# Performance work log

Measured on AMD Instinct MI355X. Metric: run time of the kernel, lower is better.

Reference implementation:

```python
import jax, jax.numpy as jnp
import numpy as np

B = 16
PATCH_NUM = 32      # L of inter branch
PATCH_SIZE = 128    # L of intra branch
WIN_SIZE = PATCH_NUM * PATCH_SIZE  # 4096
H = 8
E = 64


def setup_inputs() -> dict:
    key = jax.random.key(0)
    ks = jax.random.split(key, 6)
    return {
        "q_inter": jax.random.normal(ks[0], (B, PATCH_NUM, H, E), jnp.float32),
        "k_inter": jax.random.normal(ks[1], (B, PATCH_NUM, H, E), jnp.float32),
        "v_inter": jax.random.normal(ks[2], (B, PATCH_NUM, H, E), jnp.float32),
        "q_intra": jax.random.normal(ks[3], (B, PATCH_SIZE, H, E), jnp.float32),
        "k_intra": jax.random.normal(ks[4], (B, PATCH_SIZE, H, E), jnp.float32),
        "v_intra": jax.random.normal(ks[5], (B, PATCH_SIZE, H, E), jnp.float32),
    }


def _full_attention(q, k, v):
    # q,k,v: [B, L, H, E]; full softmax attention, scale = 1/sqrt(E)
    scale = 1.0 / jnp.sqrt(jnp.asarray(q.shape[-1], q.dtype))
    score = jnp.einsum('blhe,bshe->bhls', q, k) * scale
    att = jax.nn.softmax(score, axis=-1)  # dropout is identity in eval mode
    return jnp.einsum('bhls,bshd->blhd', att, v)


def reference(q_inter, k_inter, v_inter, q_intra, k_intra, v_intra):
    V_inter = _full_attention(q_inter, k_inter, v_inter)  # [B, patch_num, H, E]
    V_intra = _full_attention(q_intra, k_intra, v_intra)  # [B, patch_size, H, E]
    # einops repeat 'b pn h d -> b (pn ps) h d': each patch repeated ps times
    V_inter_up = jnp.repeat(V_inter, PATCH_SIZE, axis=1)  # [B, win_size, H, E]
    # einops repeat 'b ps h d -> b (ps pn) h d': each position repeated pn times
    V_intra_up = jnp.repeat(V_intra, PATCH_NUM, axis=1)   # [B, win_size, H, E]
    return V_inter_up + V_intra_up
```

## Files before the change

### kernel.cpp

```cpp
#include <hip/hip_runtime.h>


#define NH 8
#define NE 64
#define ROWSTRIDE (NH * NE)

__device__ __forceinline__ float dot4(const float4 a, const float4 b) {
    return a.x * b.x + a.y * b.y + a.z * b.z + a.w * b.w;
}

template <int L>
__global__ __launch_bounds__(256) void attn_kernel(
    const float* __restrict__ qg_, const float* __restrict__ kg_,
    const float* __restrict__ vg_, float* __restrict__ dst)
{
    constexpr int TILES = L / 32;
    constexpr int CPT   = L / 32;
    constexpr int SST   = L + 1;
    constexpr int KST   = 68;

    __shared__ __align__(16) float Ks[L * KST];
    __shared__ __align__(16) float Vs[L * KST];
    __shared__ __align__(16) float Qs[32 * KST];
    __shared__ float S[32 * SST];

    const int tid  = threadIdx.x;
    const int bid  = blockIdx.x;
    const int tile = bid % TILES;
    const int h    = (bid / TILES) % NH;
    const int b    = bid / (TILES * NH);
    const int r0   = tile * 32;

    const float* kg = kg_ + ((size_t)b * L * NH + h) * NE;
    const float* vg = vg_ + ((size_t)b * L * NH + h) * NE;
    const float* qg = qg_ + ((size_t)(b * L + r0) * NH + h) * NE;

    for (int idx = tid; idx < L * 16; idx += 256) {
        const int row = idx >> 4;
        const int f   = (idx & 15) * 4;
        *(float4*)&Ks[row * KST + f] = *(const float4*)(kg + (size_t)row * ROWSTRIDE + f);
        *(float4*)&Vs[row * KST + f] = *(const float4*)(vg + (size_t)row * ROWSTRIDE + f);
    }
    for (int idx = tid; idx < 32 * 16; idx += 256) {
        const int row = idx >> 4;
        const int f   = (idx & 15) * 4;
        *(float4*)&Qs[row * KST + f] = *(const float4*)(qg + (size_t)row * ROWSTRIDE + f);
    }
    __syncthreads();

    {
        const int rg = tid >> 5;
        const int cg = tid & 31;
        const int rr = rg * 4;
        const int c0 = cg * CPT;
        float acc[4][CPT];
        #pragma unroll
        for (int i = 0; i < 4; i++)
            #pragma unroll
            for (int j = 0; j < CPT; j++) acc[i][j] = 0.f;

        #pragma unroll
        for (int e = 0; e < NE; e += 4) {
            float4 qv[4], kv[CPT];
            #pragma unroll
            for (int i = 0; i < 4; i++) qv[i] = *(const float4*)&Qs[(rr + i) * KST + e];
            #pragma unroll
            for (int j = 0; j < CPT; j++) kv[j] = *(const float4*)&Ks[(c0 + j) * KST + e];
            #pragma unroll
            for (int i = 0; i < 4; i++)
                #pragma unroll
                for (int j = 0; j < CPT; j++)
                    acc[i][j] += dot4(qv[i], kv[j]);
        }
        #pragma unroll
        for (int i = 0; i < 4; i++)
            #pragma unroll
            for (int j = 0; j < CPT; j++)
                S[(rr + i) * SST + c0 + j] = acc[i][j] * 0.125f;
    }
    __syncthreads();

    const int r   = tid >> 3;
    const int sub = tid & 7;
    float m = -1e30f;
    for (int c = 0; c < L; c++) m = fmaxf(m, S[r * SST + c]);
    float sum = 0.f;
    for (int c = 0; c < L; c++) sum += __expf(S[r * SST + c] - m);
    const float inv = 1.f / sum;
    __syncthreads();
    for (int c = sub; c < L; c += 8)
        S[r * SST + c] = __expf(S[r * SST + c] - m);
    __syncthreads();

    const int e0 = sub * 8;
    float a0=0,a1=0,a2=0,a3=0,a4=0,a5=0,a6=0,a7=0;
    for (int c = 0; c < L; c++) {
        const float p  = S[r * SST + c];
        const float4 va = *(const float4*)&Vs[c * KST + e0];
        const float4 vb = *(const float4*)&Vs[c * KST + e0 + 4];
        a0 += p * va.x; a1 += p * va.y; a2 += p * va.z; a3 += p * va.w;
        a4 += p * vb.x; a5 += p * vb.y; a6 += p * vb.z; a7 += p * vb.w;
    }
    const float4 oA = make_float4(a0 * inv, a1 * inv, a2 * inv, a3 * inv);
    const float4 oB = make_float4(a4 * inv, a5 * inv, a6 * inv, a7 * inv);

    float* w = dst + ((size_t)(b * L + r0 + r) * NH + h) * NE + e0;
    *(float4*)w       = oA;
    *(float4*)(w + 4) = oB;
}

__global__ __launch_bounds__(256) void upsample_add_kernel(
    const float4* __restrict__ wsI, const float4* __restrict__ wsT,
    float4* __restrict__ out)
{
    const int total = 16 * 4096 * NH * (NE / 4);
    int t = blockIdx.x * 256 + threadIdx.x;
    const int stride = gridDim.x * 256;
    for (; t < total; t += stride) {
        const int e4 = t & 15;
        const int h  = (t >> 4) & 7;
        const int l  = (t >> 7) & 4095;
        const int b  = t >> 19;
        const float4 a = wsI[((b * 32  + (l >> 7)) * NH + h) * 16 + e4];
        const float4 c = wsT[((b * 128 + (l >> 5)) * NH + h) * 16 + e4];
        out[t] = make_float4(a.x + c.x, a.y + c.y, a.z + c.z, a.w + c.w);
    }
}

extern "C" void kernel_launch(void* const* d_in, const int* in_sizes, int n_in,
                              void* d_out, int out_size, void* d_ws, size_t ws_size,
                              hipStream_t stream) {
    const float* q_inter = (const float*)d_in[0];
    const float* k_inter = (const float*)d_in[1];
    const float* v_inter = (const float*)d_in[2];
    const float* q_intra = (const float*)d_in[3];
    const float* k_intra = (const float*)d_in[4];
    const float* v_intra = (const float*)d_in[5];
    float* out = (float*)d_out;
    float* wsI = (float*)d_ws;
    float* wsT = wsI + (size_t)16 * 32 * NH * NE;

    attn_kernel<32><<<16 * 8, 256, 0, stream>>>(q_inter, k_inter, v_inter, wsI);

    attn_kernel<128><<<16 * 8 * 4, 256, 0, stream>>>(q_intra, k_intra, v_intra, wsT);

    upsample_add_kernel<<<8192, 256, 0, stream>>>(
        (const float4*)wsI, (const float4*)wsT, (float4*)out);
}
```

Baseline: 194.6 us.

## Restructure upsample to one read per 32 writes and interleave K columns

The upsample kernel now gives each thread one (batch, patch, group, head, e4) pair. It computes the inter+intra sum once and stores it to the 32 consecutive output rows that share it, instead of re-reading both workspace values for every output element. This cuts redundant loads and index arithmetic in a write-bound kernel, but leaves fewer threads and more stores per thread. In the attention kernel, each thread's score columns are interleaved (cg + j*32) rather than contiguous, and V uses an unpadded stride. Both changes alter the shared-memory bank access patterns.

```diff
diff --git a/kernel.cpp b/kernel.cpp
--- a/kernel.cpp
+++ b/kernel.cpp
@@ -18,10 +18,12 @@
     constexpr int CPT   = L / 32;
     constexpr int SST   = L + 1;
     constexpr int KST   = 68;
+    constexpr int QST   = 68;
+    constexpr int VST   = 64;
 
     __shared__ __align__(16) float Ks[L * KST];
-    __shared__ __align__(16) float Vs[L * KST];
-    __shared__ __align__(16) float Qs[32 * KST];
+    __shared__ __align__(16) float Vs[L * VST];
+    __shared__ __align__(16) float Qs[32 * QST];
     __shared__ float S[32 * SST];
 
     const int tid  = threadIdx.x;
@@ -39,12 +41,12 @@
         const int row = idx >> 4;
         const int f   = (idx & 15) * 4;
         *(float4*)&Ks[row * KST + f] = *(const float4*)(kg + (size_t)row * ROWSTRIDE + f);
-        *(float4*)&Vs[row * KST + f] = *(const float4*)(vg + (size_t)row * ROWSTRIDE + f);
+        *(float4*)&Vs[row * VST + f] = *(const float4*)(vg + (size_t)row * ROWSTRIDE + f);
     }
     for (int idx = tid; idx < 32 * 16; idx += 256) {
         const int row = idx >> 4;
         const int f   = (idx & 15) * 4;
-        *(float4*)&Qs[row * KST + f] = *(const float4*)(qg + (size_t)row * ROWSTRIDE + f);
+        *(float4*)&Qs[row * QST + f] = *(const float4*)(qg + (size_t)row * ROWSTRIDE + f);
     }
     __syncthreads();
 
@@ -52,7 +54,6 @@
         const int rg = tid >> 5;
         const int cg = tid & 31;
         const int rr = rg * 4;
-        const int c0 = cg * CPT;
         float acc[4][CPT];
         #pragma unroll
         for (int i = 0; i < 4; i++)
@@ -63,9 +64,9 @@
         for (int e = 0; e < NE; e += 4) {
             float4 qv[4], kv[CPT];
             #pragma unroll
-            for (int i = 0; i < 4; i++) qv[i] = *(const float4*)&Qs[(rr + i) * KST + e];
+            for (int i = 0; i < 4; i++) qv[i] = *(const float4*)&Qs[(rr + i) * QST + e];
             #pragma unroll
-            for (int j = 0; j < CPT; j++) kv[j] = *(const float4*)&Ks[(c0 + j) * KST + e];
+            for (int j = 0; j < CPT; j++) kv[j] = *(const float4*)&Ks[(cg + j * 32) * KST + e];
             #pragma unroll
             for (int i = 0; i < 4; i++)
                 #pragma unroll
@@ -76,7 +77,7 @@
         for (int i = 0; i < 4; i++)
             #pragma unroll
             for (int j = 0; j < CPT; j++)
-                S[(rr + i) * SST + c0 + j] = acc[i][j] * 0.125f;
+                S[(rr + i) * SST + cg + j * 32] = acc[i][j] * 0.125f;
     }
     __syncthreads();
 
@@ -96,8 +97,8 @@
     float a0=0,a1=0,a2=0,a3=0,a4=0,a5=0,a6=0,a7=0;
     for (int c = 0; c < L; c++) {
         const float p  = S[r * SST + c];
-        const float4 va = *(const float4*)&Vs[c * KST + e0];
-        const float4 vb = *(const float4*)&Vs[c * KST + e0 + 4];
+        const float4 va = *(const float4*)&Vs[c * VST + e0];
+        const float4 vb = *(const float4*)&Vs[c * VST + e0 + 4];
         a0 += p * va.x; a1 += p * va.y; a2 += p * va.z; a3 += p * va.w;
         a4 += p * vb.x; a5 += p * vb.y; a6 += p * vb.z; a7 += p * vb.w;
     }
@@ -113,18 +114,21 @@
     const float4* __restrict__ wsI, const float4* __restrict__ wsT,
     float4* __restrict__ out)
 {
-    const int total = 16 * 4096 * NH * (NE / 4);
-    int t = blockIdx.x * 256 + threadIdx.x;
-    const int stride = gridDim.x * 256;
-    for (; t < total; t += stride) {
-        const int e4 = t & 15;
-        const int h  = (t >> 4) & 7;
-        const int l  = (t >> 7) & 4095;
-        const int b  = t >> 19;
-        const float4 a = wsI[((b * 32  + (l >> 7)) * NH + h) * 16 + e4];
-        const float4 c = wsT[((b * 128 + (l >> 5)) * NH + h) * 16 + e4];
-        out[t] = make_float4(a.x + c.x, a.y + c.y, a.z + c.z, a.w + c.w);
-    }
+    const int t  = blockIdx.x * 256 + threadIdx.x;
+    const int e4 = t & 15;
+    const int h  = (t >> 4) & 7;
+    const int g  = (t >> 7) & 3;
+    const int pn = (t >> 9) & 31;
+    const int b  = t >> 14;
+
+    const float4 a = wsI[((b * 32 + pn) * NH + h) * 16 + e4];
+    const float4 c = wsT[((b * 128 + pn * 4 + g) * NH + h) * 16 + e4];
+    const float4 s = make_float4(a.x + c.x, a.y + c.y, a.z + c.z, a.w + c.w);
+
+    float4* o = out + ((((size_t)b * 4096 + pn * 128 + g * 32) * NH + h) * 16 + e4);
+    #pragma unroll
+    for (int j = 0; j < 32; j++)
+        o[(size_t)j * (ROWSTRIDE / 4)] = s;
 }
 
 extern "C" void kernel_launch(void* const* d_in, const int* in_sizes, int n_in,
@@ -144,6 +148,6 @@
 
     attn_kernel<128><<<16 * 8 * 4, 256, 0, stream>>>(q_intra, k_intra, v_intra, wsT);
 
-    upsample_add_kernel<<<8192, 256, 0, stream>>>(
+    upsample_add_kernel<<<1024, 256, 0, stream>>>(
         (const float4*)wsI, (const float4*)wsT, (float4*)out);
 }
```

After: 191.2 us. Within noise of the previous version (-1.7%).
